# Optimization experiments

Measured on AMD Instinct MI355X. Metric: run time of the kernel, lower is better.

## Reference

```python
import jax, jax.numpy as jnp
import numpy as np

B, S, E, H = 2, 2048, 1024, 16
HD = E // H
DFF = 4 * E
LN_EPS = 1e-5


def _layernorm(x, g, b):
    mu = jnp.mean(x, axis=-1, keepdims=True)
    var = jnp.mean(jnp.square(x - mu), axis=-1, keepdims=True)
    return (x - mu) * jax.lax.rsqrt(var + LN_EPS) * g + b


def setup_inputs() -> dict:
    key = jax.random.key(0)
    ks = jax.random.split(key, 6)
    inp = {
        "x": jax.random.normal(ks[0], (B, S, E), jnp.float32),
        "ln1_g": jnp.ones((E,), jnp.float32),
        "ln1_b": jnp.zeros((E,), jnp.float32),
        "ln2_g": jnp.ones((E,), jnp.float32),
        "ln2_b": jnp.zeros((E,), jnp.float32),
        # OptimizedPoincareBallLinear init: randn * 0.1, zero bias
        "w_qkv": jax.random.normal(ks[1], (3 * E, E), jnp.float32) * 0.1,
        "b_qkv": jnp.zeros((3 * E,), jnp.float32),
        "w_ao": jax.random.normal(ks[2], (E, E), jnp.float32) * 0.1,
        "b_ao": jnp.zeros((E,), jnp.float32),
        "w_fc": jax.random.normal(ks[3], (DFF, E), jnp.float32) * 0.1,
        "b_fc": jnp.zeros((DFF,), jnp.float32),
        "w_po": jax.random.normal(ks[4], (E, DFF), jnp.float32) * 0.1,
        "b_po": jnp.zeros((E,), jnp.float32),
    }
    return inp


def reference(x, ln1_g, ln1_b, ln2_g, ln2_b, w_qkv, b_qkv, w_ao, b_ao,
              w_fc, b_fc, w_po, b_po):
    # --- attention branch ---
    h = _layernorm(x, ln1_g, ln1_b)
    qkv = h @ w_qkv.T + b_qkv                       # [B,S,3E]
    qkv = qkv.reshape(B, S, H, 3 * HD).transpose(0, 2, 1, 3)  # [B,H,S,3hd]
    q, k, v = jnp.split(qkv, 3, axis=-1)            # each [B,H,S,hd]
    scores = jnp.einsum('bhqd,bhkd->bhqk', q, k) / jnp.sqrt(
        jnp.asarray(HD, jnp.float32))
    causal = jnp.tril(jnp.ones((S, S), bool))        # attn_bias[:, :, :S, :S]
    scores = jnp.where(causal, scores, jnp.finfo(scores.dtype).min)
    attn_w = jax.nn.softmax(scores, axis=-1)         # dropout p=0.1 inactive (eval)
    attn = jnp.einsum('bhqk,bhkd->bhqd', attn_w, v)  # [B,H,S,hd]
    attn = attn.transpose(0, 2, 1, 3).reshape(B, S, E)
    attn = attn @ w_ao.T + b_ao
    x = x + attn
    # --- MLP branch ---
    h2 = _layernorm(x, ln2_g, ln2_b)
    h2 = h2 @ w_fc.T + b_fc
    h2 = jax.nn.gelu(h2, approximate=True)           # GPT-2 gelu_new
    h2 = h2 @ w_po.T + b_po
    x = x + h2
    return x
```

## Files before the change

### kernel.cpp

```cpp
#include <hip/hip_runtime.h>
#include <cstddef>
#include <cstdint>

#define Bc 2
#define Sc 2048
#define Ec 1024
#define Hc 16
#define HDc 64
#define DFFc 4096
#define ROWS (Bc * Sc)

typedef _Float16 half8v __attribute__((ext_vector_type(8)));
typedef _Float16 half4v __attribute__((ext_vector_type(4)));
typedef float f32x4 __attribute__((ext_vector_type(4)));
typedef _Float16 h16;

__device__ inline void gld_lds16(const void* g, void* l) {
    __builtin_amdgcn_global_load_lds(
        (const __attribute__((address_space(1))) void*)g,
        (__attribute__((address_space(3))) void*)l, 16, 0, 0);
}

__device__ inline float gelu_new(float x) {
    float x2 = x * x;
    float u = x * fmaf(0.07135481627362f, x2, 1.5957691216057308f);
    return x / (1.0f + __expf(-u));
}

__global__ __launch_bounds__(256) void cvt4_kernel(
    const float* __restrict__ a,
    const float* __restrict__ b,
    const float* __restrict__ c,
    const float* __restrict__ d,
    h16* __restrict__ out)
{
    int bid = blockIdx.x;
    const float* src;
    size_t obase;
    int base;
    if (bid < 3072)      { src = a; obase = 0;       base = bid; }
    else if (bid < 4096) { src = b; obase = 3145728; base = bid - 3072; }
    else if (bid < 8192) { src = c; obase = 4194304; base = bid - 4096; }
    else                 { src = d; obase = 8388608; base = bid - 8192; }
    int i = base * 1024 + threadIdx.x * 4;
    float4 v = *(const float4*)(src + i);
    half4v o;
    o.x = (h16)v.x; o.y = (h16)v.y; o.z = (h16)v.z; o.w = (h16)v.w;
    *(half4v*)(out + obase + i) = o;
}

__device__ inline float block_sum256(float v, float* sb) {
    #pragma unroll
    for (int o = 32; o > 0; o >>= 1) v += __shfl_down(v, o, 64);
    int lane = threadIdx.x & 63, w = threadIdx.x >> 6;
    if (lane == 0) sb[w] = v;
    __syncthreads();
    float r = sb[0] + sb[1] + sb[2] + sb[3];
    __syncthreads();
    return r;
}

__global__ __launch_bounds__(256) void ln_kernel(const float* __restrict__ x,
                                                 const float* __restrict__ g,
                                                 const float* __restrict__ b,
                                                 h16* __restrict__ out) {
    __shared__ float sb[4];
    int row = blockIdx.x;
    int t = threadIdx.x;
    const float* xr = x + (size_t)row * Ec;
    float4 v = ((const float4*)xr)[t];
    float s = v.x + v.y + v.z + v.w;
    float mu = block_sum256(s, sb) * (1.0f / Ec);
    float dx = v.x - mu, dy = v.y - mu, dz = v.z - mu, dw = v.w - mu;
    float ss = dx * dx + dy * dy + dz * dz + dw * dw;
    float var = block_sum256(ss, sb) * (1.0f / Ec);
    float inv = rsqrtf(var + 1e-5f);
    float4 gv = ((const float4*)g)[t];
    float4 bv = ((const float4*)b)[t];
    half4v o;
    o.x = (h16)(dx * inv * gv.x + bv.x);
    o.y = (h16)(dy * inv * gv.y + bv.y);
    o.z = (h16)(dz * inv * gv.z + bv.z);
    o.w = (h16)(dw * inv * gv.w + bv.w);
    ((half4v*)(out + (size_t)row * Ec))[t] = o;
}

template <int EPI, typename OutT>
__global__ __launch_bounds__(256) void gemm_mfma(
    const h16* __restrict__ A, const h16* __restrict__ W,
    const float* __restrict__ bias, const float* __restrict__ R,
    OutT* __restrict__ C, int M, int N, int K)
{
    __shared__ h16 As[2][128 * 32];
    __shared__ h16 Ws[2][128 * 32];

    const int t = threadIdx.x;
    const int lane = t & 63, wv = t >> 6;
    const int wm = wv >> 1, wn = wv & 1;
    const int c15 = lane & 15, q = lane >> 4;
    const int row0 = blockIdx.y * 128, col0 = blockIdx.x * 128;
    const int arow = t >> 2, acol = (t & 3) << 3;

    const h16* ap0 = A + (size_t)(row0 + arow) * K + acol;
    const h16* ap1 = ap0 + (size_t)64 * K;
    const h16* wp0 = W + (size_t)(col0 + arow) * K + acol;
    const h16* wp1 = wp0 + (size_t)64 * K;

    f32x4 acc[4][4];
    #pragma unroll
    for (int i = 0; i < 4; ++i)
        #pragma unroll
        for (int j = 0; j < 4; ++j)
            acc[i][j] = (f32x4){0.f, 0.f, 0.f, 0.f};

    auto stageL = [&](h16* asB, h16* wsB, int koff) {
        gld_lds16(ap0 + koff, asB + arow * 32 + acol);
        gld_lds16(ap1 + koff, asB + (64 + arow) * 32 + acol);
        gld_lds16(wp0 + koff, wsB + arow * 32 + acol);
        gld_lds16(wp1 + koff, wsB + (64 + arow) * 32 + acol);
    };
    auto computeL = [&](const h16* asB, const h16* wsB) {
        half8v af[4], bfv[4];
        #pragma unroll
        for (int i = 0; i < 4; ++i)
            af[i] = *(const half8v*)&asB[(wm * 64 + i * 16 + c15) * 32 + q * 8];
        #pragma unroll
        for (int j = 0; j < 4; ++j)
            bfv[j] = *(const half8v*)&wsB[(wn * 64 + j * 16 + c15) * 32 + q * 8];
        #pragma unroll
        for (int i = 0; i < 4; ++i)
            #pragma unroll
            for (int j = 0; j < 4; ++j)
                acc[i][j] = __builtin_amdgcn_mfma_f32_16x16x32_f16(af[i], bfv[j], acc[i][j], 0, 0, 0);
    };

    stageL(As[0], Ws[0], 0);
    __syncthreads();

    int k0 = 0;
    for (; k0 < K - 64; k0 += 64) {
        stageL(As[1], Ws[1], k0 + 32);
        computeL(As[0], Ws[0]);
        __syncthreads();
        stageL(As[0], Ws[0], k0 + 64);
        computeL(As[1], Ws[1]);
        __syncthreads();
    }
    stageL(As[1], Ws[1], k0 + 32);
    computeL(As[0], Ws[0]);
    __syncthreads();
    computeL(As[1], Ws[1]);

    #pragma unroll
    for (int i = 0; i < 4; ++i) {
        #pragma unroll
        for (int j = 0; j < 4; ++j) {
            int col = col0 + wn * 64 + j * 16 + c15;
            float bv = bias[col];
            #pragma unroll
            for (int r = 0; r < 4; ++r) {
                int row = row0 + wm * 64 + i * 16 + q * 4 + r;
                size_t off = (size_t)row * N + col;
                float v = acc[i][j][r] + bv;
                if (EPI == 1) v += R[off];
                if (EPI == 2) v = gelu_new(v);
                if (sizeof(OutT) == 2) ((h16*)C)[off] = (h16)v;
                else ((float*)C)[off] = v;
            }
        }
    }
}

template <int EPI, typename OutT>
__global__ __launch_bounds__(256) void gemm_k64(
    const h16* __restrict__ A, const h16* __restrict__ W,
    const float* __restrict__ bias, const float* __restrict__ R,
    OutT* __restrict__ C, int M, int N, int K)
{
    __shared__ h16 As[2][2][64 * 32];
    __shared__ h16 Ws[2][2][128 * 32];

    const int t = threadIdx.x;
    const int lane = t & 63, wv = t >> 6;
    const int wm = wv >> 1, wn = wv & 1;
    const int c15 = lane & 15, q = lane >> 4;
    const int id = blockIdx.x;
    const int cx = id & 7;
    const int kq = id >> 3;
    const int bx = kq & 7;
    const int by = ((kq >> 3) << 3) | cx;
    const int row0 = by * 64, col0 = bx * 128;
    const int arow = t >> 2, acol = (t & 3) << 3;

    const h16* ap  = A + (size_t)(row0 + arow) * K + acol;
    const h16* wp0 = W + (size_t)(col0 + arow) * K + acol;
    const h16* wp1 = wp0 + (size_t)64 * K;

    f32x4 acc[2][4];
    #pragma unroll
    for (int i = 0; i < 2; ++i)
        #pragma unroll
        for (int j = 0; j < 4; ++j)
            acc[i][j] = (f32x4){0.f, 0.f, 0.f, 0.f};

    auto stageL = [&](h16 (*asB)[64 * 32], h16 (*wsB)[128 * 32], int koff) {
        #pragma unroll
        for (int kk = 0; kk < 2; ++kk) {
            gld_lds16(ap  + koff + kk * 32, &asB[kk][arow * 32 + acol]);
            gld_lds16(wp0 + koff + kk * 32, &wsB[kk][arow * 32 + acol]);
            gld_lds16(wp1 + koff + kk * 32, &wsB[kk][(64 + arow) * 32 + acol]);
        }
    };
    auto computeL = [&](const h16 (*asB)[64 * 32], const h16 (*wsB)[128 * 32]) {
        #pragma unroll
        for (int kk = 0; kk < 2; ++kk) {
            half8v af[2], bfv[4];
            #pragma unroll
            for (int i = 0; i < 2; ++i)
                af[i] = *(const half8v*)&asB[kk][(wm * 32 + i * 16 + c15) * 32 + q * 8];
            #pragma unroll
            for (int j = 0; j < 4; ++j)
                bfv[j] = *(const half8v*)&wsB[kk][(wn * 64 + j * 16 + c15) * 32 + q * 8];
            #pragma unroll
            for (int i = 0; i < 2; ++i)
                #pragma unroll
                for (int j = 0; j < 4; ++j)
                    acc[i][j] = __builtin_amdgcn_mfma_f32_16x16x32_f16(af[i], bfv[j], acc[i][j], 0, 0, 0);
        }
    };

    stageL(As[0], Ws[0], 0);
    __syncthreads();

    int k0 = 0;
    for (; k0 < K - 128; k0 += 128) {
        stageL(As[1], Ws[1], k0 + 64);
        computeL(As[0], Ws[0]);
        __syncthreads();
        stageL(As[0], Ws[0], k0 + 128);
        computeL(As[1], Ws[1]);
        __syncthreads();
    }
    stageL(As[1], Ws[1], k0 + 64);
    computeL(As[0], Ws[0]);
    __syncthreads();
    computeL(As[1], Ws[1]);

    #pragma unroll
    for (int i = 0; i < 2; ++i) {
        #pragma unroll
        for (int j = 0; j < 4; ++j) {
            int col = col0 + wn * 64 + j * 16 + c15;
            float bv = bias[col];
            #pragma unroll
            for (int r = 0; r < 4; ++r) {
                int row = row0 + wm * 32 + i * 16 + q * 4 + r;
                size_t off = (size_t)row * N + col;
                float v = acc[i][j][r] + bv;
                if (EPI == 1) v += R[off];
                if (EPI == 2) v = gelu_new(v);
                if (sizeof(OutT) == 2) ((h16*)C)[off] = (h16)v;
                else ((float*)C)[off] = v;
            }
        }
    }
}

__global__ __launch_bounds__(256, 4) void attn_mfma(const h16* __restrict__ qkv,
                                                    h16* __restrict__ attn) {
    __shared__ h16 Ks[2][2][64 * 32];
    __shared__ h16 Vt[2][64 * 32];
    __shared__ h16 Ps[4][16 * 72];

    const int t = threadIdx.x;
    const int lane = t & 63, wv = t >> 6;
    const int c15 = lane & 15, q = lane >> 4;
    const int bh = blockIdx.x, b = bh >> 4, h = bh & 15;
    const int ja = 31 - blockIdx.y;
    const int qbase = ja * 64 + wv * 16;
    const int SE = 3 * Ec;
    const size_t hbase = (size_t)b * Sc * SE + (size_t)h * (3 * HDc);

    half8v qf[2];
    #pragma unroll
    for (int kk = 0; kk < 2; ++kk) {
        qf[kk] = *(const half8v*)(qkv + hbase + (size_t)(qbase + c15) * SE + kk * 32 + q * 8);
        qf[kk] *= (h16)0.125f;
    }

    f32x4 O[4];
    #pragma unroll
    for (int n = 0; n < 4; ++n) O[n] = (f32x4){0.f, 0.f, 0.f, 0.f};
    float mi = -3e38f, li = 0.f;

    const int krow = t >> 2, kcol = (t & 3) << 3;
    const int vkey = t & 31, vd0 = (t >> 5) << 3;
    half8v vreg[2];

    auto stageK = [&](int kt, int bf) {
        #pragma unroll
        for (int p = 0; p < 2; ++p)
            gld_lds16(qkv + hbase + (size_t)(kt * 64 + krow) * SE + HDc + p * 32 + kcol,
                      &Ks[bf][p][krow * 32 + kcol]);
    };
    auto loadV = [&](int kt) {
        #pragma unroll
        for (int p = 0; p < 2; ++p)
            vreg[p] = *(const half8v*)(qkv + hbase +
                        (size_t)(kt * 64 + p * 32 + vkey) * SE + 2 * HDc + vd0);
    };
    auto scatV = [&]() {
        #pragma unroll
        for (int p = 0; p < 2; ++p)
            #pragma unroll
            for (int u = 0; u < 8; ++u)
                Vt[p][(vd0 + u) * 32 + vkey] = vreg[p][u];
    };

    stageK(0, 0);
    loadV(0);
    scatV();
    __syncthreads();

    for (int kt = 0; kt <= ja; ++kt) {
        const int bf = kt & 1;
        if (kt < ja) { stageK(kt + 1, bf ^ 1); loadV(kt + 1); }

        f32x4 st[4];
        #pragma unroll
        for (int j = 0; j < 4; ++j) {
            half8v kf0 = *(const half8v*)&Ks[bf][0][(j * 16 + c15) * 32 + q * 8];
            half8v kf1 = *(const half8v*)&Ks[bf][1][(j * 16 + c15) * 32 + q * 8];
            f32x4 z = (f32x4){0.f, 0.f, 0.f, 0.f};
            z = __builtin_amdgcn_mfma_f32_16x16x32_f16(kf0, qf[0], z, 0, 0, 0);
            st[j] = __builtin_amdgcn_mfma_f32_16x16x32_f16(kf1, qf[1], z, 0, 0, 0);
        }

        if (kt == ja) {
            const int rowloc = wv * 16 + c15;
            #pragma unroll
            for (int j = 0; j < 4; ++j)
                #pragma unroll
                for (int r = 0; r < 4; ++r)
                    if (j * 16 + q * 4 + r > rowloc) st[j][r] = -3e38f;
        }

        float mx = mi;
        #pragma unroll
        for (int j = 0; j < 4; ++j)
            #pragma unroll
            for (int r = 0; r < 4; ++r) mx = fmaxf(mx, st[j][r]);
        mx = fmaxf(mx, __shfl_xor(mx, 16, 64));
        mx = fmaxf(mx, __shfl_xor(mx, 32, 64));
        float al = __expf(mi - mx);
        mi = mx;
        float ps = 0.f;
        #pragma unroll
        for (int j = 0; j < 4; ++j) {
            half4v pk;
            #pragma unroll
            for (int r = 0; r < 4; ++r) {
                float p = __expf(st[j][r] - mx);
                ps += p;
                pk[r] = (h16)p;
            }
            *(half4v*)&Ps[wv][c15 * 72 + j * 16 + q * 4] = pk;
        }
        ps += __shfl_xor(ps, 16, 64);
        ps += __shfl_xor(ps, 32, 64);
        li = li * al + ps;

        half8v pb0 = *(const half8v*)&Ps[wv][c15 * 72 + q * 8];
        half8v pb1 = *(const half8v*)&Ps[wv][c15 * 72 + 32 + q * 8];
        #pragma unroll
        for (int n = 0; n < 4; ++n) {
            #pragma unroll
            for (int r = 0; r < 4; ++r) O[n][r] *= al;
            half8v va0 = *(const half8v*)&Vt[0][(n * 16 + c15) * 32 + q * 8];
            half8v va1 = *(const half8v*)&Vt[1][(n * 16 + c15) * 32 + q * 8];
            O[n] = __builtin_amdgcn_mfma_f32_16x16x32_f16(va0, pb0, O[n], 0, 0, 0);
            O[n] = __builtin_amdgcn_mfma_f32_16x16x32_f16(va1, pb1, O[n], 0, 0, 0);
        }

        if (kt < ja) {
            __syncthreads();
            scatV();
            __syncthreads();
        }
    }

    float rl = 1.0f / li;
    #pragma unroll
    for (int n = 0; n < 4; ++n) {
        half4v o4;
        #pragma unroll
        for (int r = 0; r < 4; ++r) o4[r] = (h16)(O[n][r] * rl);
        *(half4v*)(attn + ((size_t)(b * Sc + qbase + c15)) * Ec + h * HDc + n * 16 + q * 4) = o4;
    }
}

extern "C" void kernel_launch(void* const* d_in, const int* in_sizes, int n_in,
                              void* d_out, int out_size, void* d_ws, size_t ws_size,
                              hipStream_t stream) {
    const float* x     = (const float*)d_in[0];
    const float* ln1_g = (const float*)d_in[1];
    const float* ln1_b = (const float*)d_in[2];
    const float* ln2_g = (const float*)d_in[3];
    const float* ln2_b = (const float*)d_in[4];
    const float* w_qkv = (const float*)d_in[5];
    const float* b_qkv = (const float*)d_in[6];
    const float* w_ao  = (const float*)d_in[7];
    const float* b_ao  = (const float*)d_in[8];
    const float* w_fc  = (const float*)d_in[9];
    const float* b_fc  = (const float*)d_in[10];
    const float* w_po  = (const float*)d_in[11];
    const float* b_po  = (const float*)d_in[12];
    float* out = (float*)d_out;

    char* w = (char*)d_ws;
    h16* wqkv = (h16*)(w);
    h16* wao  = (h16*)(w + 6291456);
    h16* wfc  = (h16*)(w + 8388608);
    h16* wpo  = (h16*)(w + 16777216);
    h16* hb   = (h16*)(w + 25165824);
    h16* qkv  = (h16*)(w + 33554432);
    h16* attn = (h16*)(w + 58720256);
    float* x1 = (float*)(w + 67108864);
    h16* ff   = qkv;

    dim3 blk(256);

    cvt4_kernel<<<dim3(12288), blk, 0, stream>>>(w_qkv, w_ao, w_fc, w_po, wqkv);

    ln_kernel<<<dim3(ROWS), blk, 0, stream>>>(x, ln1_g, ln1_b, hb);
    gemm_mfma<0, h16><<<dim3(3 * Ec / 128, ROWS / 128), blk, 0, stream>>>(
        hb, wqkv, b_qkv, nullptr, qkv, ROWS, 3 * Ec, Ec);
    attn_mfma<<<dim3(Bc * Hc, 32), blk, 0, stream>>>(qkv, attn);
    gemm_k64<1, float><<<dim3(512), blk, 0, stream>>>(
        attn, wao, b_ao, x, x1, ROWS, Ec, Ec);
    ln_kernel<<<dim3(ROWS), blk, 0, stream>>>(x1, ln2_g, ln2_b, hb);
    gemm_mfma<2, h16><<<dim3(DFFc / 128, ROWS / 128), blk, 0, stream>>>(
        hb, wfc, b_fc, nullptr, ff, ROWS, DFFc, Ec);
    gemm_k64<1, float><<<dim3(512), blk, 0, stream>>>(
        ff, wpo, b_po, x1, out, ROWS, Ec, DFFc);
}
```

Baseline: 351.9 us.

## Replace QKV and FC GEMMs with 256x256 eight-wave kernel using 4-stage LDS pipeline

The 128x128 four-wave GEMM for the QKV and FC projections is replaced by a 256x256-tile, 512-thread kernel. It keeps four LDS buffers with three tiles in flight, paced by explicit vmcnt waits and raw barriers, and uses an XOR swizzle to avoid LDS bank conflicts. Blocks are remapped across the 8 XCDs for L2 locality, and the MFMA section runs at raised wave priority. The larger tile improves operand reuse and hides load latency better, at the cost of 128 accumulator registers per thread, 128 KB of LDS, and fewer blocks (192 for QKV, 256 for FC), which may leave some CUs idle.

```diff
diff --git a/kernel.cpp b/kernel.cpp
--- a/kernel.cpp
+++ b/kernel.cpp
@@ -86,82 +86,102 @@
 }
 
 template <int EPI, typename OutT>
-__global__ __launch_bounds__(256) void gemm_mfma(
+__global__ __launch_bounds__(512, 2) void gemm_8w(
     const h16* __restrict__ A, const h16* __restrict__ W,
     const float* __restrict__ bias, const float* __restrict__ R,
     OutT* __restrict__ C, int M, int N, int K)
 {
-    __shared__ h16 As[2][128 * 32];
-    __shared__ h16 Ws[2][128 * 32];
-
-    const int t = threadIdx.x;
-    const int lane = t & 63, wv = t >> 6;
-    const int wm = wv >> 1, wn = wv & 1;
+    __shared__ h16 S[4][16384];
+
+    const int tid = threadIdx.x;
+    const int lane = tid & 63, wv = tid >> 6;
+    const int wm = wv >> 2, wn = wv & 3;
     const int c15 = lane & 15, q = lane >> 4;
-    const int row0 = blockIdx.y * 128, col0 = blockIdx.x * 128;
-    const int arow = t >> 2, acol = (t & 3) << 3;
-
-    const h16* ap0 = A + (size_t)(row0 + arow) * K + acol;
-    const h16* ap1 = ap0 + (size_t)64 * K;
-    const h16* wp0 = W + (size_t)(col0 + arow) * K + acol;
-    const h16* wp1 = wp0 + (size_t)64 * K;
-
-    f32x4 acc[4][4];
-    #pragma unroll
-    for (int i = 0; i < 4; ++i)
-        #pragma unroll
-        for (int j = 0; j < 4; ++j)
-            acc[i][j] = (f32x4){0.f, 0.f, 0.f, 0.f};
-
-    auto stageL = [&](h16* asB, h16* wsB, int koff) {
-        gld_lds16(ap0 + koff, asB + arow * 32 + acol);
-        gld_lds16(ap1 + koff, asB + (64 + arow) * 32 + acol);
-        gld_lds16(wp0 + koff, wsB + arow * 32 + acol);
-        gld_lds16(wp1 + koff, wsB + (64 + arow) * 32 + acol);
-    };
-    auto computeL = [&](const h16* asB, const h16* wsB) {
-        half8v af[4], bfv[4];
-        #pragma unroll
-        for (int i = 0; i < 4; ++i)
-            af[i] = *(const half8v*)&asB[(wm * 64 + i * 16 + c15) * 32 + q * 8];
-        #pragma unroll
-        for (int j = 0; j < 4; ++j)
-            bfv[j] = *(const half8v*)&wsB[(wn * 64 + j * 16 + c15) * 32 + q * 8];
-        #pragma unroll
-        for (int i = 0; i < 4; ++i)
-            #pragma unroll
-            for (int j = 0; j < 4; ++j)
-                acc[i][j] = __builtin_amdgcn_mfma_f32_16x16x32_f16(af[i], bfv[j], acc[i][j], 0, 0, 0);
-    };
-
-    stageL(As[0], Ws[0], 0);
-    __syncthreads();
-
-    int k0 = 0;
-    for (; k0 < K - 64; k0 += 64) {
-        stageL(As[1], Ws[1], k0 + 32);
-        computeL(As[0], Ws[0]);
-        __syncthreads();
-        stageL(As[0], Ws[0], k0 + 64);
-        computeL(As[1], Ws[1]);
-        __syncthreads();
-    }
-    stageL(As[1], Ws[1], k0 + 32);
-    computeL(As[0], Ws[0]);
-    __syncthreads();
-    computeL(As[1], Ws[1]);
-
-    #pragma unroll
-    for (int i = 0; i < 4; ++i) {
-        #pragma unroll
-        for (int j = 0; j < 4; ++j) {
-            int col = col0 + wn * 64 + j * 16 + c15;
-            float bv = bias[col];
+
+    const int nbn = N >> 8;
+    const int cpx = gridDim.x >> 3;
+    const int wg = ((int)blockIdx.x & 7) * cpx + ((int)blockIdx.x >> 3);
+    const int r0 = (wg / nbn) << 8, c0 = (wg % nbn) << 8;
+
+    const int gc8 = (tid & 3) ^ ((tid >> 3) & 3);
+    const h16* gA = A + (size_t)(r0 + (tid >> 2)) * K + gc8 * 8;
+    const h16* gB = W + (size_t)(c0 + (tid >> 2)) * K + gc8 * 8;
+    const size_t hK = (size_t)128 * K;
+
+    int aoff[8], boff[4];
+    #pragma unroll
+    for (int m = 0; m < 8; ++m) {
+        int row = wm * 128 + m * 16 + c15;
+        aoff[m] = row * 32 + ((q ^ ((row >> 1) & 3)) << 3);
+    }
+    #pragma unroll
+    for (int n = 0; n < 4; ++n) {
+        int row = wn * 64 + n * 16 + c15;
+        boff[n] = 8192 + row * 32 + ((q ^ ((row >> 1) & 3)) << 3);
+    }
+
+    f32x4 acc[8][4];
+    #pragma unroll
+    for (int m = 0; m < 8; ++m)
+        #pragma unroll
+        for (int n = 0; n < 4; ++n)
+            acc[m][n] = (f32x4){0.f, 0.f, 0.f, 0.f};
+
+    const int NT = K >> 5;
+
+    auto stage = [&](int tt) {
+        h16* b = &S[tt & 3][0];
+        const h16* a = gA + tt * 32;
+        const h16* w = gB + tt * 32;
+        gld_lds16(a,      b + tid * 8);
+        gld_lds16(a + hK, b + 4096 + tid * 8);
+        gld_lds16(w,      b + 8192 + tid * 8);
+        gld_lds16(w + hK, b + 12288 + tid * 8);
+    };
+
+    stage(0); stage(1); stage(2);
+    asm volatile("s_waitcnt vmcnt(8)" ::: "memory");
+    __builtin_amdgcn_s_barrier();
+
+    for (int t = 0; t < NT; ++t) {
+        if (t + 3 < NT) stage(t + 3);
+
+        const h16* b = &S[t & 3][0];
+        half8v af[8], bf[4];
+        #pragma unroll
+        for (int m = 0; m < 8; ++m) af[m] = *(const half8v*)(b + aoff[m]);
+        #pragma unroll
+        for (int n = 0; n < 4; ++n) bf[n] = *(const half8v*)(b + boff[n]);
+
+        __builtin_amdgcn_s_setprio(1);
+        #pragma unroll
+        for (int m = 0; m < 8; ++m)
+            #pragma unroll
+            for (int n = 0; n < 4; ++n)
+                acc[m][n] = __builtin_amdgcn_mfma_f32_16x16x32_f16(af[m], bf[n], acc[m][n], 0, 0, 0);
+        __builtin_amdgcn_s_setprio(0);
+
+        if (t < NT - 1) {
+            if (t + 3 < NT)       asm volatile("s_waitcnt vmcnt(8)" ::: "memory");
+            else if (t + 3 == NT) asm volatile("s_waitcnt vmcnt(4)" ::: "memory");
+            else                  asm volatile("s_waitcnt vmcnt(0)" ::: "memory");
+            __builtin_amdgcn_s_barrier();
+        }
+    }
+
+    float bvs[4];
+    #pragma unroll
+    for (int n = 0; n < 4; ++n) bvs[n] = bias[c0 + wn * 64 + n * 16 + c15];
+    #pragma unroll
+    for (int m = 0; m < 8; ++m) {
+        #pragma unroll
+        for (int n = 0; n < 4; ++n) {
+            int col = c0 + wn * 64 + n * 16 + c15;
             #pragma unroll
             for (int r = 0; r < 4; ++r) {
-                int row = row0 + wm * 64 + i * 16 + q * 4 + r;
+                int row = r0 + wm * 128 + m * 16 + q * 4 + r;
                 size_t off = (size_t)row * N + col;
-                float v = acc[i][j][r] + bv;
+                float v = acc[m][n][r] + bvs[n];
                 if (EPI == 1) v += R[off];
                 if (EPI == 2) v = gelu_new(v);
                 if (sizeof(OutT) == 2) ((h16*)C)[off] = (h16)v;
@@ -429,17 +449,18 @@
     h16* ff   = qkv;
 
     dim3 blk(256);
+    dim3 blk8(512);
 
     cvt4_kernel<<<dim3(12288), blk, 0, stream>>>(w_qkv, w_ao, w_fc, w_po, wqkv);
 
     ln_kernel<<<dim3(ROWS), blk, 0, stream>>>(x, ln1_g, ln1_b, hb);
-    gemm_mfma<0, h16><<<dim3(3 * Ec / 128, ROWS / 128), blk, 0, stream>>>(
+    gemm_8w<0, h16><<<dim3((ROWS / 256) * (3 * Ec / 256)), blk8, 0, stream>>>(
         hb, wqkv, b_qkv, nullptr, qkv, ROWS, 3 * Ec, Ec);
     attn_mfma<<<dim3(Bc * Hc, 32), blk, 0, stream>>>(qkv, attn);
     gemm_k64<1, float><<<dim3(512), blk, 0, stream>>>(
         attn, wao, b_ao, x, x1, ROWS, Ec, Ec);
     ln_kernel<<<dim3(ROWS), blk, 0, stream>>>(x1, ln2_g, ln2_b, hb);
-    gemm_mfma<2, h16><<<dim3(DFFc / 128, ROWS / 128), blk, 0, stream>>>(
+    gemm_8w<2, h16><<<dim3((ROWS / 256) * (DFFc / 256)), blk8, 0, stream>>>(
         hb, wfc, b_fc, nullptr, ff, ROWS, DFFc, Ec);
     gemm_k64<1, float><<<dim3(512), blk, 0, stream>>>(
         ff, wpo, b_po, x1, out, ROWS, Ec, DFFc);
```

Result: faster. 332.6 us (-5.5%).
